# Optimization experiments

Measured on AMD Instinct MI355X. Metric: run time of the kernel, lower is better.

Reference implementation:

```python
import jax, jax.numpy as jnp
import numpy as np

P = 7            # cfg.POOLING_SIZE (= group_size)
N_CLASSES = 21   # PASCAL VOC incl. background
SPATIAL_SCALE = 1.0 / 16.0


def _round_half_up(x):
    # matches C round() for non-negative roi coords (jnp.round is banker's)
    return jnp.floor(x + 0.5)


def psroi_pool(feat, rois, out_dim):
    """Position-sensitive RoI average pooling via integral images.
    feat: [B, out_dim*P*P, H, W]; rois: [N, 5] (batch_idx, x1, y1, x2, y2).
    Returns [N, out_dim, P, P]."""
    B, C, H, W = feat.shape
    # summed-area table, zero-padded: S[b,c,h,w] = sum feat[b,c,:h,:w]
    S = jnp.cumsum(jnp.cumsum(feat, axis=2), axis=3)
    S = jnp.pad(S, ((0, 0), (0, 0), (1, 0), (1, 0)))

    b = rois[:, 0].astype(jnp.int32)
    x1 = _round_half_up(rois[:, 1]) * SPATIAL_SCALE
    y1 = _round_half_up(rois[:, 2]) * SPATIAL_SCALE
    x2 = _round_half_up(rois[:, 3] + 1.0) * SPATIAL_SCALE
    y2 = _round_half_up(rois[:, 4] + 1.0) * SPATIAL_SCALE
    roi_w = jnp.maximum(x2 - x1, 0.1)
    roi_h = jnp.maximum(y2 - y1, 0.1)
    bin_w = roi_w / P
    bin_h = roi_h / P

    g = jnp.arange(P, dtype=feat.dtype)
    hs = jnp.clip(jnp.floor(g[None] * bin_h[:, None] + y1[:, None]), 0, H).astype(jnp.int32)        # [N,P]
    he = jnp.clip(jnp.ceil((g[None] + 1.0) * bin_h[:, None] + y1[:, None]), 0, H).astype(jnp.int32)
    ws = jnp.clip(jnp.floor(g[None] * bin_w[:, None] + x1[:, None]), 0, W).astype(jnp.int32)
    we = jnp.clip(jnp.ceil((g[None] + 1.0) * bin_w[:, None] + x1[:, None]), 0, W).astype(jnp.int32)

    # channel for (ctop, gh, gw) is (ctop*P + gh)*P + gw == arange(C) reshaped
    c = jnp.arange(C, dtype=jnp.int32).reshape(1, out_dim, P, P)
    bi = b[:, None, None, None]
    h0 = hs[:, None, :, None]; h1 = he[:, None, :, None]
    w0 = ws[:, None, None, :]; w1 = we[:, None, None, :]
    # box-sum from integral image -> [N, out_dim, P, P]
    ssum = S[bi, c, h1, w1] - S[bi, c, h0, w1] - S[bi, c, h1, w0] + S[bi, c, h0, w0]

    dh = jnp.maximum(he - hs, 0)[:, None, :, None]
    dw = jnp.maximum(we - ws, 0)[:, None, None, :]
    area = (dh * dw).astype(feat.dtype)
    return jnp.where(area > 0, ssum / jnp.maximum(area, 1.0), 0.0)


def setup_inputs() -> dict:
    key = jax.random.key(0)
    k1, k2, k3, k4, k5 = jax.random.split(key, 5)
    B, Cin, H, W = 4, 2048, 64, 64
    base_feat = jax.random.normal(k1, (B, Cin, H, W), jnp.float32)
    w_conv1 = 0.01 * jax.random.normal(k2, (1024, Cin), jnp.float32)
    w_cls = 0.01 * jax.random.normal(k3, (N_CLASSES * P * P, 1024), jnp.float32)
    w_bbox = 0.001 * jax.random.normal(k4, (4 * N_CLASSES * P * P, 1024), jnp.float32)
    # 300 ROIs per image in image coords (image size = 16*H = 1024)
    n_per = 300
    ka, kb = jax.random.split(k5)
    xy1 = jax.random.uniform(ka, (B * n_per, 2), jnp.float32, 0.0, 900.0)
    wh = jax.random.uniform(kb, (B * n_per, 2), jnp.float32, 16.0, 160.0)
    xy2 = jnp.minimum(xy1 + wh, 1023.0)
    bidx = jnp.repeat(jnp.arange(B, dtype=jnp.float32), n_per)[:, None]
    rois = jnp.concatenate([bidx, xy1[:, 0:1], xy1[:, 1:2], xy2[:, 0:1], xy2[:, 1:2]], axis=1)
    return {"base_feat": base_feat, "rois": rois, "w_conv1": w_conv1, "w_cls": w_cls, "w_bbox": w_bbox}


def reference(base_feat, rois, w_conv1, w_cls, w_bbox):
    B = base_feat.shape[0]
    n_per = rois.shape[0] // B
    # 1x1 conv (no bias) + relu
    x = jax.nn.relu(jnp.einsum('oi,bihw->bohw', w_conv1, base_feat))
    # cls branch: 1x1 conv -> PSRoIPool -> PxP avgpool -> softmax
    cls_feat = jnp.einsum('oi,bihw->bohw', w_cls, x)
    pooled_cls = psroi_pool(cls_feat, rois, N_CLASSES)        # [N, 21, P, P]
    cls_score = pooled_cls.mean(axis=(2, 3))                   # [N, 21]
    cls_prob = jax.nn.softmax(cls_score, axis=1)
    # bbox branch: 1x1 conv -> PSRoIPool -> PxP avgpool
    bbox_feat = jnp.einsum('oi,bihw->bohw', w_bbox, x)
    pooled_loc = psroi_pool(bbox_feat, rois, 4 * N_CLASSES)    # [N, 84, P, P]
    bbox_pred = pooled_loc.mean(axis=(2, 3))                    # [N, 84]
    return cls_prob.reshape(B, n_per, -1), bbox_pred.reshape(B, n_per, -1)
```

## Files before the change

kernel.cpp:

```cpp
#include <hip/hip_runtime.h>
#include <cstdint>


typedef __attribute__((ext_vector_type(8))) short short8;
typedef __attribute__((ext_vector_type(4))) short short4v;
typedef __attribute__((ext_vector_type(4))) float f32x4;

#define OFF_FEATT 0ull
#define OFF_W1    67108864ull
#define OFF_U2    0ull
#define OFF_P2    64225280ull
#define OFF_WC    71303168ull
#define OFF_DESC  84148224ull
#define OFF_SCORE 86155264ull
#define OFF_X     86810624ull
#define OFF_U1    153919488ull
#define OFF_P1    282370048ull
#define ONEPASS_BYTES 296419328ull

__device__ __forceinline__ unsigned short f2bf(float f) {
  unsigned u = __float_as_uint(f);
  u += 0x7fffu + ((u >> 16) & 1u);
  return (unsigned short)(u >> 16);
}
__device__ __forceinline__ float bf2f(unsigned short h) {
  return __uint_as_float(((unsigned)h) << 16);
}

__device__ __forceinline__ int swz6(int k6, int key) {
  return ((((k6 >> 3) & 7) ^ key) << 3) | (k6 & 7);
}

__device__ __forceinline__ void gload16(const void* g, void* l) {
  __builtin_amdgcn_global_load_lds((const __attribute__((address_space(1))) void*)g,
                                   (__attribute__((address_space(3))) void*)l, 16, 0, 0);
}

__global__ __launch_bounds__(256) void k_cvt_w1(const float* __restrict__ src,
                                                unsigned short* __restrict__ dst) {
  int t = blockIdx.x * 256 + threadIdx.x;
  long e = (long)t * 4;
  if (e >= 1024 * 2048) return;
  int o = (int)(e >> 11), k = (int)(e & 2047);
  float4 q = *(const float4*)(src + e);
  short4v s = {(short)f2bf(q.x), (short)f2bf(q.y), (short)f2bf(q.z), (short)f2bf(q.w)};
  int kp = (k & ~63) | swz6(k & 63, o & 7);
  *(short4v*)(dst + (size_t)o * 2048 + kp) = s;
}

__global__ __launch_bounds__(256) void k_cvt_wcomb(const float* __restrict__ wcls,
                                                   const float* __restrict__ wbbox,
                                                   unsigned short* __restrict__ dst) {
  int t = blockIdx.x * 256 + threadIdx.x;
  if (t >= 128 * 49 * 256) return;
  size_t e = (size_t)t * 4;
  int c = (int)(e / 50176);
  int rem = (int)(e - (size_t)c * 50176);
  int ij = rem >> 10, k = rem & 1023;
  float4 q = make_float4(0.f, 0.f, 0.f, 0.f);
  if (c < 21)       q = *(const float4*)(wcls + (size_t)(c * 49 + ij) * 1024 + k);
  else if (c < 105) q = *(const float4*)(wbbox + (size_t)((c - 21) * 49 + ij) * 1024 + k);
  short4v s = {(short)f2bf(q.x), (short)f2bf(q.y), (short)f2bf(q.z), (short)f2bf(q.w)};
  int kp = (k & ~63) | swz6(k & 63, c & 7);
  *(short4v*)(dst + ((size_t)(c * 49 + ij) * 1024 + kp)) = s;
}

__global__ __launch_bounds__(256) void k_tpose(const float* __restrict__ src,
                                               unsigned short* __restrict__ dst) {
  __shared__ float tile[64][65];
  int s0 = blockIdx.x * 64, c0 = blockIdx.y * 64, b = blockIdx.z;
  int tx = threadIdx.x & 63, ty = threadIdx.x >> 6;
  const float* sp = src + ((size_t)b * 2048 + c0) * 4096 + s0;
#pragma unroll
  for (int i = 0; i < 16; i++) {
    int cl = ty * 16 + i;
    tile[cl][tx] = sp[(size_t)cl * 4096 + tx];
  }
  __syncthreads();
  unsigned short* dp = dst + ((size_t)b * 4096 + s0) * 2048 + c0;
  int c4 = (threadIdx.x & 15) * 4;
  int sy = threadIdx.x >> 4;
#pragma unroll
  for (int i = 0; i < 4; i++) {
    int sl = i * 16 + sy;
    int key = sl & 7;
    short4v v = {(short)f2bf(tile[c4 + 0][sl]), (short)f2bf(tile[c4 + 1][sl]),
                 (short)f2bf(tile[c4 + 2][sl]), (short)f2bf(tile[c4 + 3][sl])};
    *(short4v*)(dp + (size_t)sl * 2048 + swz6(c4, key)) = v;
  }
}

__global__ __launch_bounds__(256) void k_gemm_conv1(const short* __restrict__ A,
                                                    const short* __restrict__ Bw,
                                                    float* __restrict__ X) {
  int mt = blockIdx.x, nt = blockIdx.y, b = blockIdx.z;
  __shared__ short As[128 * 64];
  __shared__ short Bs[128 * 64];
  int tid = threadIdx.x, lane = tid & 63, wave = tid >> 6;
  int wm = wave >> 1, wn = wave & 1;
  f32x4 acc[4][4];
#pragma unroll
  for (int i = 0; i < 4; i++)
#pragma unroll
    for (int j = 0; j < 4; j++) acc[i][j] = (f32x4){0.f, 0.f, 0.f, 0.f};

  const short* Ab = A + ((size_t)b * 4096 + (size_t)mt * 128) * 2048;
  const short* Bb = Bw + (size_t)nt * 128 * 2048;
  int lr = lane >> 3;
  int lc = (lane & 7) * 8;
  int key = lane & 7;

  for (int k0 = 0; k0 < 2048; k0 += 64) {
#pragma unroll
    for (int i = 0; i < 4; i++) {
      int row = i * 32 + wave * 8 + lr;
      gload16(Ab + (size_t)row * 2048 + k0 + lc, (char*)As + (i * 32 + wave * 8) * 128);
      gload16(Bb + (size_t)row * 2048 + k0 + lc, (char*)Bs + (i * 32 + wave * 8) * 128);
    }
    __syncthreads();
#pragma unroll
    for (int kt = 0; kt < 2; kt++) {
      int ko = (((kt << 2) | (lane >> 4)) ^ key) << 3;
      short8 af[4], bfr[4];
#pragma unroll
      for (int i = 0; i < 4; i++)
        af[i] = *(const short8*)(As + (wm * 64 + i * 16 + (lane & 15)) * 64 + ko);
#pragma unroll
      for (int j = 0; j < 4; j++)
        bfr[j] = *(const short8*)(Bs + (wn * 64 + j * 16 + (lane & 15)) * 64 + ko);
#pragma unroll
      for (int i = 0; i < 4; i++)
#pragma unroll
        for (int j = 0; j < 4; j++)
          acc[i][j] = __builtin_amdgcn_mfma_f32_16x16x32_bf16(af[i], bfr[j], acc[i][j], 0, 0, 0);
    }
    __syncthreads();
  }
  float* Xb = X + ((size_t)b * 4096 + (size_t)mt * 128) * 1024 + nt * 128;
#pragma unroll
  for (int i = 0; i < 4; i++)
#pragma unroll
    for (int j = 0; j < 4; j++) {
      int row = wm * 64 + i * 16 + (lane >> 4) * 4;
      int col = wn * 64 + j * 16 + (lane & 15);
#pragma unroll
      for (int r = 0; r < 4; r++)
        Xb[(size_t)(row + r) * 1024 + col] = fmaxf(acc[i][j][r], 0.f);
    }
}

__global__ __launch_bounds__(256) void k_desc(const float* __restrict__ rois,
                                              int* __restrict__ desc) {
  int t = blockIdx.x * 256 + threadIdx.x;
  if (t >= 1280 * 49) return;
  int roi = t / 49, ij = t - roi * 49;
  int* d = desc + (size_t)t * 8;
  if (roi >= 1200) { d[0] = 0; d[1] = 0; d[2] = 0; d[3] = 0; d[4] = 0; ((float*)d)[5] = 0.f; return; }
  const float* r = rois + (size_t)roi * 5;
  int b = (int)r[0];
  float x1 = __fmul_rn(floorf(__fadd_rn(r[1], 0.5f)), 0.0625f);
  float y1 = __fmul_rn(floorf(__fadd_rn(r[2], 0.5f)), 0.0625f);
  float x2 = __fmul_rn(floorf(__fadd_rn(__fadd_rn(r[3], 1.0f), 0.5f)), 0.0625f);
  float y2 = __fmul_rn(floorf(__fadd_rn(__fadd_rn(r[4], 1.0f), 0.5f)), 0.0625f);
  float bw = __fdiv_rn(fmaxf(__fsub_rn(x2, x1), 0.1f), 7.0f);
  float bh = __fdiv_rn(fmaxf(__fsub_rn(y2, y1), 0.1f), 7.0f);
  int i = ij / 7, j = ij - (ij / 7) * 7;
  float fi = (float)i, fj = (float)j;
  int hs = (int)fminf(fmaxf(floorf(__fadd_rn(__fmul_rn(fi, bh), y1)), 0.f), 64.f);
  int he = (int)fminf(fmaxf(ceilf(__fadd_rn(__fmul_rn(__fadd_rn(fi, 1.f), bh), y1)), 0.f), 64.f);
  int wsx = (int)fminf(fmaxf(floorf(__fadd_rn(__fmul_rn(fj, bw), x1)), 0.f), 64.f);
  int we = (int)fminf(fmaxf(ceilf(__fadd_rn(__fmul_rn(__fadd_rn(fj, 1.f), bw), x1)), 0.f), 64.f);
  int dh = max(he - hs, 0), dw = max(we - wsx, 0);
  float inv = (dh * dw > 0) ? 1.0f / (float)(dh * dw) : 0.f;
  d[0] = b; d[1] = hs; d[2] = he; d[3] = wsx; d[4] = we;
  ((float*)d)[5] = inv;
}

__global__ __launch_bounds__(256) void k_ubuild(const float* __restrict__ X,
                                                const int* __restrict__ desc,
                                                unsigned short* __restrict__ U) {
  int t = blockIdx.x;
  const int* d = desc + (size_t)t * 8;
  int b = d[0], hs = d[1], he = d[2], wsx = d[3], we = d[4];
  float inv = ((const float*)d)[5];
  int key = (t / 49) & 7;
  int k = threadIdx.x * 4;
  float ax = 0.f, ay = 0.f, az = 0.f, aw = 0.f;
  for (int h = hs; h < he; h++) {
    const float* rowp = X + ((size_t)((b * 64 + h) * 64 + wsx)) * 1024 + k;
    for (int w = wsx; w < we; w++) {
      float4 q = *(const float4*)rowp;
      ax += q.x; ay += q.y; az += q.z; aw += q.w;
      rowp += 1024;
    }
  }
  short4v s = {(short)f2bf(ax * inv), (short)f2bf(ay * inv),
               (short)f2bf(az * inv), (short)f2bf(aw * inv)};
  int kp = (k & ~63) | swz6(k & 63, key);
  *(short4v*)(U + (size_t)t * 1024 + kp) = s;
}

__global__ __launch_bounds__(256) void k_poolgemm2(const unsigned short* __restrict__ U,
                                                   const unsigned short* __restrict__ Wc,
                                                   unsigned short* __restrict__ P,
                                                   int nroi) {
  int mt = blockIdx.x;
  int ij = blockIdx.y;
  __shared__ short As[64 * 64];
  __shared__ short Bs[128 * 64];
  int tid = threadIdx.x, lane = tid & 63, wave = tid >> 6;
  f32x4 acc[4][2];
#pragma unroll
  for (int i = 0; i < 4; i++)
#pragma unroll
    for (int j = 0; j < 2; j++) acc[i][j] = (f32x4){0.f, 0.f, 0.f, 0.f};

  const unsigned short* Ab = U + ((size_t)mt * 64 * 49 + ij) * 1024;
  const unsigned short* Bb = Wc + (size_t)ij * 1024;
  int lr = lane >> 3, lc = (lane & 7) * 8;
  int key = lane & 7;

  for (int k0 = 0; k0 < 1024; k0 += 64) {
#pragma unroll
    for (int i = 0; i < 2; i++) {
      int row = i * 32 + wave * 8 + lr;
      gload16(Ab + (size_t)row * (49 * 1024) + k0 + lc, (char*)As + (i * 32 + wave * 8) * 128);
    }
#pragma unroll
    for (int i = 0; i < 4; i++) {
      int row = i * 32 + wave * 8 + lr;
      gload16(Bb + (size_t)row * (49 * 1024) + k0 + lc, (char*)Bs + (i * 32 + wave * 8) * 128);
    }
    __syncthreads();
#pragma unroll
    for (int kt = 0; kt < 2; kt++) {
      int ko = (((kt << 2) | (lane >> 4)) ^ key) << 3;
      short8 af[4], bfr[2];
#pragma unroll
      for (int i = 0; i < 4; i++)
        af[i] = *(const short8*)(As + (i * 16 + (lane & 15)) * 64 + ko);
#pragma unroll
      for (int j = 0; j < 2; j++)
        bfr[j] = *(const short8*)(Bs + (wave * 32 + j * 16 + (lane & 15)) * 64 + ko);
#pragma unroll
      for (int i = 0; i < 4; i++)
#pragma unroll
        for (int j = 0; j < 2; j++)
          acc[i][j] = __builtin_amdgcn_mfma_f32_16x16x32_bf16(af[i], bfr[j], acc[i][j], 0, 0, 0);
    }
    __syncthreads();
  }
  unsigned short* Pb = P + (size_t)ij * nroi * 112;
#pragma unroll
  for (int i = 0; i < 4; i++)
#pragma unroll
    for (int j = 0; j < 2; j++) {
      int cc = wave * 32 + j * 16 + (lane & 15);
      if (cc < 112) {
        int rbase = mt * 64 + i * 16 + (lane >> 4) * 4;
#pragma unroll
        for (int r = 0; r < 4; r++)
          Pb[(size_t)(rbase + r) * 112 + cc] = f2bf(acc[i][j][r]);
      }
    }
}

__global__ __launch_bounds__(256) void k_reduce(const unsigned short* __restrict__ P,
                                                float* __restrict__ score, int nroi) {
  int t = blockIdx.x * 256 + threadIdx.x;
  if (t >= nroi * 112) return;
  int roi = t / 112, c = t - roi * 112;
  float s = 0.f;
#pragma unroll 7
  for (int ij = 0; ij < 49; ij++) s += bf2f(P[(size_t)ij * nroi * 112 + t]);
  score[(size_t)roi * 128 + c] = s;
}

__global__ __launch_bounds__(256) void k_final(const float* __restrict__ score,
                                               float* __restrict__ out) {
  int t = blockIdx.x * 256 + threadIdx.x;
  if (t < 1200) {
    float s[21];
    float mx = -1e30f;
#pragma unroll
    for (int c = 0; c < 21; c++) {
      s[c] = score[(size_t)t * 128 + c] * (1.f / 49.f);
      mx = fmaxf(mx, s[c]);
    }
    float sum = 0.f;
#pragma unroll
    for (int c = 0; c < 21; c++) { s[c] = expf(s[c] - mx); sum += s[c]; }
    float rs = 1.f / sum;
#pragma unroll
    for (int c = 0; c < 21; c++) out[(size_t)t * 21 + c] = s[c] * rs;
  }
  if (t < 100800) {
    int roi = t / 84, c = t - (t / 84) * 84;
    out[25200 + t] = score[(size_t)roi * 128 + 21 + c] * (1.f / 49.f);
  }
}

extern "C" void kernel_launch(void* const* d_in, const int* in_sizes, int n_in,
                              void* d_out, int out_size, void* d_ws, size_t ws_size,
                              hipStream_t stream) {
  const float* base_feat = (const float*)d_in[0];
  const float* rois      = (const float*)d_in[1];
  const float* w_conv1   = (const float*)d_in[2];
  const float* w_cls     = (const float*)d_in[3];
  const float* w_bbox    = (const float*)d_in[4];
  float* out = (float*)d_out;
  char* ws = (char*)d_ws;

  unsigned short* featT = (unsigned short*)(ws + OFF_FEATT);
  unsigned short* w1b   = (unsigned short*)(ws + OFF_W1);
  unsigned short* Wc    = (unsigned short*)(ws + OFF_WC);
  int*            desc  = (int*)(ws + OFF_DESC);
  float*          score = (float*)(ws + OFF_SCORE);
  float*          X     = (float*)(ws + OFF_X);

  k_cvt_w1<<<2048, 256, 0, stream>>>(w_conv1, w1b);
  k_cvt_wcomb<<<6272, 256, 0, stream>>>(w_cls, w_bbox, Wc);
  k_tpose<<<dim3(64, 32, 4), 256, 0, stream>>>(base_feat, featT);
  k_gemm_conv1<<<dim3(32, 8, 4), 256, 0, stream>>>((const short*)featT, (const short*)w1b, X);
  k_desc<<<245, 256, 0, stream>>>(rois, desc);

  if (ws_size >= ONEPASS_BYTES) {
    unsigned short* U = (unsigned short*)(ws + OFF_U1);
    unsigned short* P = (unsigned short*)(ws + OFF_P1);
    k_ubuild<<<1280 * 49, 256, 0, stream>>>(X, desc, U);
    k_poolgemm2<<<dim3(20, 49), 256, 0, stream>>>(U, Wc, P, 1280);
    k_reduce<<<560, 256, 0, stream>>>(P, score, 1280);
  } else {
    unsigned short* U = (unsigned short*)(ws + OFF_U2);
    unsigned short* P = (unsigned short*)(ws + OFF_P2);
    for (int h = 0; h < 2; h++) {
      k_ubuild<<<640 * 49, 256, 0, stream>>>(X, desc + (size_t)h * 640 * 49 * 8, U);
      k_poolgemm2<<<dim3(10, 49), 256, 0, stream>>>(U, Wc, P, 640);
      k_reduce<<<280, 256, 0, stream>>>(P, score + (size_t)h * 640 * 128, 640);
    }
  }
  k_final<<<394, 256, 0, stream>>>(score, out);
}
```

Before: 434.6 us.

## Fuse RoI bin gathering into pool GEMM and merge prep kernels

Removes the separate U buffer: the pool GEMM now gathers and averages X over each RoI bin directly into a double-buffered LDS A tile, and prefetches the next weight tile while gathering. The three small prep kernels (weight conversions, descriptor build) merge into one launch, and the two-pass fallback path is dropped. This avoids writing and re-reading a large bf16 intermediate and cuts launch count. The cost is a longer-latency gather inside the GEMM loop, with lower occupancy from doubled LDS, and each thread now does scattered gathers.

```diff
diff --git a/kernel.cpp b/kernel.cpp
--- a/kernel.cpp
+++ b/kernel.cpp
@@ -7,16 +7,12 @@
 typedef __attribute__((ext_vector_type(4))) float f32x4;
 
 #define OFF_FEATT 0ull
+#define OFF_P     0ull
 #define OFF_W1    67108864ull
-#define OFF_U2    0ull
-#define OFF_P2    64225280ull
 #define OFF_WC    71303168ull
 #define OFF_DESC  84148224ull
 #define OFF_SCORE 86155264ull
 #define OFF_X     86810624ull
-#define OFF_U1    153919488ull
-#define OFF_P1    282370048ull
-#define ONEPASS_BYTES 296419328ull
 
 __device__ __forceinline__ unsigned short f2bf(float f) {
   unsigned u = __float_as_uint(f);
@@ -36,122 +32,37 @@
                                    (__attribute__((address_space(3))) void*)l, 16, 0, 0);
 }
 
-__global__ __launch_bounds__(256) void k_cvt_w1(const float* __restrict__ src,
-                                                unsigned short* __restrict__ dst) {
-  int t = blockIdx.x * 256 + threadIdx.x;
-  long e = (long)t * 4;
-  if (e >= 1024 * 2048) return;
-  int o = (int)(e >> 11), k = (int)(e & 2047);
-  float4 q = *(const float4*)(src + e);
-  short4v s = {(short)f2bf(q.x), (short)f2bf(q.y), (short)f2bf(q.z), (short)f2bf(q.w)};
-  int kp = (k & ~63) | swz6(k & 63, o & 7);
-  *(short4v*)(dst + (size_t)o * 2048 + kp) = s;
-}
-
-__global__ __launch_bounds__(256) void k_cvt_wcomb(const float* __restrict__ wcls,
-                                                   const float* __restrict__ wbbox,
-                                                   unsigned short* __restrict__ dst) {
-  int t = blockIdx.x * 256 + threadIdx.x;
-  if (t >= 128 * 49 * 256) return;
-  size_t e = (size_t)t * 4;
-  int c = (int)(e / 50176);
-  int rem = (int)(e - (size_t)c * 50176);
-  int ij = rem >> 10, k = rem & 1023;
-  float4 q = make_float4(0.f, 0.f, 0.f, 0.f);
-  if (c < 21)       q = *(const float4*)(wcls + (size_t)(c * 49 + ij) * 1024 + k);
-  else if (c < 105) q = *(const float4*)(wbbox + (size_t)((c - 21) * 49 + ij) * 1024 + k);
-  short4v s = {(short)f2bf(q.x), (short)f2bf(q.y), (short)f2bf(q.z), (short)f2bf(q.w)};
-  int kp = (k & ~63) | swz6(k & 63, c & 7);
-  *(short4v*)(dst + ((size_t)(c * 49 + ij) * 1024 + kp)) = s;
-}
-
-__global__ __launch_bounds__(256) void k_tpose(const float* __restrict__ src,
-                                               unsigned short* __restrict__ dst) {
-  __shared__ float tile[64][65];
-  int s0 = blockIdx.x * 64, c0 = blockIdx.y * 64, b = blockIdx.z;
-  int tx = threadIdx.x & 63, ty = threadIdx.x >> 6;
-  const float* sp = src + ((size_t)b * 2048 + c0) * 4096 + s0;
-#pragma unroll
-  for (int i = 0; i < 16; i++) {
-    int cl = ty * 16 + i;
-    tile[cl][tx] = sp[(size_t)cl * 4096 + tx];
-  }
-  __syncthreads();
-  unsigned short* dp = dst + ((size_t)b * 4096 + s0) * 2048 + c0;
-  int c4 = (threadIdx.x & 15) * 4;
-  int sy = threadIdx.x >> 4;
-#pragma unroll
-  for (int i = 0; i < 4; i++) {
-    int sl = i * 16 + sy;
-    int key = sl & 7;
-    short4v v = {(short)f2bf(tile[c4 + 0][sl]), (short)f2bf(tile[c4 + 1][sl]),
-                 (short)f2bf(tile[c4 + 2][sl]), (short)f2bf(tile[c4 + 3][sl])};
-    *(short4v*)(dp + (size_t)sl * 2048 + swz6(c4, key)) = v;
-  }
-}
-
-__global__ __launch_bounds__(256) void k_gemm_conv1(const short* __restrict__ A,
-                                                    const short* __restrict__ Bw,
-                                                    float* __restrict__ X) {
-  int mt = blockIdx.x, nt = blockIdx.y, b = blockIdx.z;
-  __shared__ short As[128 * 64];
-  __shared__ short Bs[128 * 64];
-  int tid = threadIdx.x, lane = tid & 63, wave = tid >> 6;
-  int wm = wave >> 1, wn = wave & 1;
-  f32x4 acc[4][4];
-#pragma unroll
-  for (int i = 0; i < 4; i++)
-#pragma unroll
-    for (int j = 0; j < 4; j++) acc[i][j] = (f32x4){0.f, 0.f, 0.f, 0.f};
-
-  const short* Ab = A + ((size_t)b * 4096 + (size_t)mt * 128) * 2048;
-  const short* Bb = Bw + (size_t)nt * 128 * 2048;
-  int lr = lane >> 3;
-  int lc = (lane & 7) * 8;
-  int key = lane & 7;
-
-  for (int k0 = 0; k0 < 2048; k0 += 64) {
-#pragma unroll
-    for (int i = 0; i < 4; i++) {
-      int row = i * 32 + wave * 8 + lr;
-      gload16(Ab + (size_t)row * 2048 + k0 + lc, (char*)As + (i * 32 + wave * 8) * 128);
-      gload16(Bb + (size_t)row * 2048 + k0 + lc, (char*)Bs + (i * 32 + wave * 8) * 128);
-    }
-    __syncthreads();
-#pragma unroll
-    for (int kt = 0; kt < 2; kt++) {
-      int ko = (((kt << 2) | (lane >> 4)) ^ key) << 3;
-      short8 af[4], bfr[4];
-#pragma unroll
-      for (int i = 0; i < 4; i++)
-        af[i] = *(const short8*)(As + (wm * 64 + i * 16 + (lane & 15)) * 64 + ko);
-#pragma unroll
-      for (int j = 0; j < 4; j++)
-        bfr[j] = *(const short8*)(Bs + (wn * 64 + j * 16 + (lane & 15)) * 64 + ko);
-#pragma unroll
-      for (int i = 0; i < 4; i++)
-#pragma unroll
-        for (int j = 0; j < 4; j++)
-          acc[i][j] = __builtin_amdgcn_mfma_f32_16x16x32_bf16(af[i], bfr[j], acc[i][j], 0, 0, 0);
-    }
-    __syncthreads();
-  }
-  float* Xb = X + ((size_t)b * 4096 + (size_t)mt * 128) * 1024 + nt * 128;
-#pragma unroll
-  for (int i = 0; i < 4; i++)
-#pragma unroll
-    for (int j = 0; j < 4; j++) {
-      int row = wm * 64 + i * 16 + (lane >> 4) * 4;
-      int col = wn * 64 + j * 16 + (lane & 15);
-#pragma unroll
-      for (int r = 0; r < 4; r++)
-        Xb[(size_t)(row + r) * 1024 + col] = fmaxf(acc[i][j][r], 0.f);
-    }
-}
-
-__global__ __launch_bounds__(256) void k_desc(const float* __restrict__ rois,
+__global__ __launch_bounds__(256) void k_prep(const float* __restrict__ w1,
+                                              const float* __restrict__ wcls,
+                                              const float* __restrict__ wbbox,
+                                              const float* __restrict__ rois,
+                                              unsigned short* __restrict__ w1b,
+                                              unsigned short* __restrict__ Wc,
                                               int* __restrict__ desc) {
-  int t = blockIdx.x * 256 + threadIdx.x;
+  int bid = blockIdx.x;
+  if (bid < 2048) {
+    long e = ((long)bid * 256 + threadIdx.x) * 4;
+    int o = (int)(e >> 11), k = (int)(e & 2047);
+    float4 q = *(const float4*)(w1 + e);
+    short4v s = {(short)f2bf(q.x), (short)f2bf(q.y), (short)f2bf(q.z), (short)f2bf(q.w)};
+    int kp = (k & ~63) | swz6(k & 63, o & 7);
+    *(short4v*)(w1b + (size_t)o * 2048 + kp) = s;
+    return;
+  }
+  if (bid < 8320) {
+    size_t e = ((size_t)(bid - 2048) * 256 + threadIdx.x) * 4;
+    int c = (int)(e / 50176);
+    int rem = (int)(e - (size_t)c * 50176);
+    int ij = rem >> 10, k = rem & 1023;
+    float4 q = make_float4(0.f, 0.f, 0.f, 0.f);
+    if (c < 21)       q = *(const float4*)(wcls + (size_t)(c * 49 + ij) * 1024 + k);
+    else if (c < 105) q = *(const float4*)(wbbox + (size_t)((c - 21) * 49 + ij) * 1024 + k);
+    short4v s = {(short)f2bf(q.x), (short)f2bf(q.y), (short)f2bf(q.z), (short)f2bf(q.w)};
+    int kp = (k & ~63) | swz6(k & 63, c & 7);
+    *(short4v*)(Wc + ((size_t)(c * 49 + ij) * 1024 + kp)) = s;
+    return;
+  }
+  int t = (bid - 8320) * 256 + threadIdx.x;
   if (t >= 1280 * 49) return;
   int roi = t / 49, ij = t - roi * 49;
   int* d = desc + (size_t)t * 8;
@@ -176,81 +87,188 @@
   ((float*)d)[5] = inv;
 }
 
-__global__ __launch_bounds__(256) void k_ubuild(const float* __restrict__ X,
-                                                const int* __restrict__ desc,
-                                                unsigned short* __restrict__ U) {
-  int t = blockIdx.x;
-  const int* d = desc + (size_t)t * 8;
+__global__ __launch_bounds__(256) void k_tpose(const float* __restrict__ src,
+                                               unsigned short* __restrict__ dst) {
+  __shared__ float tile[64][65];
+  int s0 = blockIdx.x * 64, c0 = blockIdx.y * 64, b = blockIdx.z;
+  int tx = threadIdx.x & 63, ty = threadIdx.x >> 6;
+  const float* sp = src + ((size_t)b * 2048 + c0) * 4096 + s0;
+#pragma unroll
+  for (int i = 0; i < 16; i++) {
+    int cl = ty * 16 + i;
+    tile[cl][tx] = sp[(size_t)cl * 4096 + tx];
+  }
+  __syncthreads();
+  unsigned short* dp = dst + ((size_t)b * 4096 + s0) * 2048 + c0;
+  int c4 = (threadIdx.x & 15) * 4;
+  int sy = threadIdx.x >> 4;
+#pragma unroll
+  for (int i = 0; i < 4; i++) {
+    int sl = i * 16 + sy;
+    int key = sl & 7;
+    short4v v = {(short)f2bf(tile[c4 + 0][sl]), (short)f2bf(tile[c4 + 1][sl]),
+                 (short)f2bf(tile[c4 + 2][sl]), (short)f2bf(tile[c4 + 3][sl])};
+    *(short4v*)(dp + (size_t)sl * 2048 + swz6(c4, key)) = v;
+  }
+}
+
+__global__ __launch_bounds__(256) void k_gemm_conv1(const short* __restrict__ A,
+                                                    const short* __restrict__ Bw,
+                                                    float* __restrict__ X) {
+  int mt = blockIdx.x, nt = blockIdx.y, b = blockIdx.z;
+  __shared__ short As[128 * 64];
+  __shared__ short Bs[128 * 64];
+  int tid = threadIdx.x, lane = tid & 63, wave = tid >> 6;
+  int wm = wave >> 1, wn = wave & 1;
+  f32x4 acc[4][4];
+#pragma unroll
+  for (int i = 0; i < 4; i++)
+#pragma unroll
+    for (int j = 0; j < 4; j++) acc[i][j] = (f32x4){0.f, 0.f, 0.f, 0.f};
+
+  const short* Ab = A + ((size_t)b * 4096 + (size_t)mt * 128) * 2048;
+  const short* Bb = Bw + (size_t)nt * 128 * 2048;
+  int lr = lane >> 3;
+  int lc = (lane & 7) * 8;
+  int key = lane & 7;
+
+  for (int k0 = 0; k0 < 2048; k0 += 64) {
+#pragma unroll
+    for (int i = 0; i < 4; i++) {
+      int row = i * 32 + wave * 8 + lr;
+      gload16(Ab + (size_t)row * 2048 + k0 + lc, (char*)As + (i * 32 + wave * 8) * 128);
+      gload16(Bb + (size_t)row * 2048 + k0 + lc, (char*)Bs + (i * 32 + wave * 8) * 128);
+    }
+    __syncthreads();
+#pragma unroll
+    for (int kt = 0; kt < 2; kt++) {
+      int ko = (((kt << 2) | (lane >> 4)) ^ key) << 3;
+      short8 af[4], bfr[4];
+#pragma unroll
+      for (int i = 0; i < 4; i++)
+        af[i] = *(const short8*)(As + (wm * 64 + i * 16 + (lane & 15)) * 64 + ko);
+#pragma unroll
+      for (int j = 0; j < 4; j++)
+        bfr[j] = *(const short8*)(Bs + (wn * 64 + j * 16 + (lane & 15)) * 64 + ko);
+#pragma unroll
+      for (int i = 0; i < 4; i++)
+#pragma unroll
+        for (int j = 0; j < 4; j++)
+          acc[i][j] = __builtin_amdgcn_mfma_f32_16x16x32_bf16(af[i], bfr[j], acc[i][j], 0, 0, 0);
+    }
+    __syncthreads();
+  }
+  float* Xb = X + ((size_t)b * 4096 + (size_t)mt * 128) * 1024 + nt * 128;
+#pragma unroll
+  for (int i = 0; i < 4; i++)
+#pragma unroll
+    for (int j = 0; j < 4; j++) {
+      int row = wm * 64 + i * 16 + (lane >> 4) * 4;
+      int col = wn * 64 + j * 16 + (lane & 15);
+#pragma unroll
+      for (int r = 0; r < 4; r++)
+        Xb[(size_t)(row + r) * 1024 + col] = fmaxf(acc[i][j][r], 0.f);
+    }
+}
+
+__global__ __launch_bounds__(256, 3) void k_poolfused(const float* __restrict__ X,
+                                                      const int* __restrict__ desc,
+                                                      const unsigned short* __restrict__ Wc,
+                                                      unsigned short* __restrict__ P) {
+  int mt = blockIdx.x;
+  int ij = blockIdx.y;
+  __shared__ short As[2][64 * 72];
+  __shared__ short Bs[2][128 * 64];
+  int tid = threadIdx.x, lane = tid & 63, wave = tid >> 6;
+  int r = tid >> 2, q = tid & 3;
+
+  const int* d = desc + ((size_t)(mt * 64 + r) * 49 + ij) * 8;
   int b = d[0], hs = d[1], he = d[2], wsx = d[3], we = d[4];
   float inv = ((const float*)d)[5];
-  int key = (t / 49) & 7;
-  int k = threadIdx.x * 4;
-  float ax = 0.f, ay = 0.f, az = 0.f, aw = 0.f;
-  for (int h = hs; h < he; h++) {
-    const float* rowp = X + ((size_t)((b * 64 + h) * 64 + wsx)) * 1024 + k;
-    for (int w = wsx; w < we; w++) {
-      float4 q = *(const float4*)rowp;
-      ax += q.x; ay += q.y; az += q.z; aw += q.w;
-      rowp += 1024;
-    }
-  }
-  short4v s = {(short)f2bf(ax * inv), (short)f2bf(ay * inv),
-               (short)f2bf(az * inv), (short)f2bf(aw * inv)};
-  int kp = (k & ~63) | swz6(k & 63, key);
-  *(short4v*)(U + (size_t)t * 1024 + kp) = s;
-}
-
-__global__ __launch_bounds__(256) void k_poolgemm2(const unsigned short* __restrict__ U,
-                                                   const unsigned short* __restrict__ Wc,
-                                                   unsigned short* __restrict__ P,
-                                                   int nroi) {
-  int mt = blockIdx.x;
-  int ij = blockIdx.y;
-  __shared__ short As[64 * 64];
-  __shared__ short Bs[128 * 64];
-  int tid = threadIdx.x, lane = tid & 63, wave = tid >> 6;
+  const float* Xq = X + (size_t)q * 16;
+
+  const unsigned short* Bb = Wc + (size_t)ij * 1024 +
+                             (size_t)(wave * 8 + (lane >> 3)) * 49 * 1024 + (lane & 7) * 8;
+  int key = lane & 7;
+
   f32x4 acc[4][2];
 #pragma unroll
   for (int i = 0; i < 4; i++)
 #pragma unroll
     for (int j = 0; j < 2; j++) acc[i][j] = (f32x4){0.f, 0.f, 0.f, 0.f};
 
-  const unsigned short* Ab = U + ((size_t)mt * 64 * 49 + ij) * 1024;
-  const unsigned short* Bb = Wc + (size_t)ij * 1024;
-  int lr = lane >> 3, lc = (lane & 7) * 8;
-  int key = lane & 7;
-
-  for (int k0 = 0; k0 < 1024; k0 += 64) {
-#pragma unroll
-    for (int i = 0; i < 2; i++) {
-      int row = i * 32 + wave * 8 + lr;
-      gload16(Ab + (size_t)row * (49 * 1024) + k0 + lc, (char*)As + (i * 32 + wave * 8) * 128);
-    }
-#pragma unroll
-    for (int i = 0; i < 4; i++) {
-      int row = i * 32 + wave * 8 + lr;
-      gload16(Bb + (size_t)row * (49 * 1024) + k0 + lc, (char*)Bs + (i * 32 + wave * 8) * 128);
+  float s[16];
+
+  auto gather = [&](int k0) {
+#pragma unroll
+    for (int z = 0; z < 16; z++) s[z] = 0.f;
+    for (int h = hs; h < he; h++) {
+      const float* rp = Xq + ((size_t)((b * 64 + h) * 64 + wsx)) * 1024 + k0;
+      for (int w = wsx; w < we; w++) {
+        float4 a0 = *(const float4*)(rp + 0);
+        float4 a1 = *(const float4*)(rp + 4);
+        float4 a2 = *(const float4*)(rp + 8);
+        float4 a3 = *(const float4*)(rp + 12);
+        s[0] += a0.x; s[1] += a0.y; s[2] += a0.z; s[3] += a0.w;
+        s[4] += a1.x; s[5] += a1.y; s[6] += a1.z; s[7] += a1.w;
+        s[8] += a2.x; s[9] += a2.y; s[10] += a2.z; s[11] += a2.w;
+        s[12] += a3.x; s[13] += a3.y; s[14] += a3.z; s[15] += a3.w;
+        rp += 1024;
+      }
+    }
+  };
+  auto writeA = [&](int buf) {
+    short8 v0 = {(short)f2bf(s[0] * inv), (short)f2bf(s[1] * inv),
+                 (short)f2bf(s[2] * inv), (short)f2bf(s[3] * inv),
+                 (short)f2bf(s[4] * inv), (short)f2bf(s[5] * inv),
+                 (short)f2bf(s[6] * inv), (short)f2bf(s[7] * inv)};
+    short8 v1 = {(short)f2bf(s[8] * inv), (short)f2bf(s[9] * inv),
+                 (short)f2bf(s[10] * inv), (short)f2bf(s[11] * inv),
+                 (short)f2bf(s[12] * inv), (short)f2bf(s[13] * inv),
+                 (short)f2bf(s[14] * inv), (short)f2bf(s[15] * inv)};
+    *(short8*)&As[buf][r * 72 + q * 16] = v0;
+    *(short8*)&As[buf][r * 72 + q * 16 + 8] = v1;
+  };
+  auto loadB = [&](int k0, int buf) {
+#pragma unroll
+    for (int i = 0; i < 4; i++)
+      gload16(Bb + (size_t)(i * 32) * 49 * 1024 + k0,
+              (char*)Bs[buf] + (i * 32 + wave * 8) * 128);
+  };
+
+  gather(0);
+  loadB(0, 0);
+  __syncthreads();
+  writeA(0);
+
+  for (int kc = 0; kc < 16; kc++) {
+    int cur = kc & 1;
+    if (kc < 15) {
+      loadB((kc + 1) * 64, cur ^ 1);
+      gather((kc + 1) * 64);
     }
     __syncthreads();
 #pragma unroll
     for (int kt = 0; kt < 2; kt++) {
-      int ko = (((kt << 2) | (lane >> 4)) ^ key) << 3;
+      int ko = kt * 32 + (lane >> 4) * 8;
+      int kob = (((kt << 2) | (lane >> 4)) ^ key) << 3;
       short8 af[4], bfr[2];
 #pragma unroll
       for (int i = 0; i < 4; i++)
-        af[i] = *(const short8*)(As + (i * 16 + (lane & 15)) * 64 + ko);
+        af[i] = *(const short8*)(&As[cur][(i * 16 + (lane & 15)) * 72 + ko]);
 #pragma unroll
       for (int j = 0; j < 2; j++)
-        bfr[j] = *(const short8*)(Bs + (wave * 32 + j * 16 + (lane & 15)) * 64 + ko);
+        bfr[j] = *(const short8*)(&Bs[cur][(wave * 32 + j * 16 + (lane & 15)) * 64 + kob]);
 #pragma unroll
       for (int i = 0; i < 4; i++)
 #pragma unroll
         for (int j = 0; j < 2; j++)
           acc[i][j] = __builtin_amdgcn_mfma_f32_16x16x32_bf16(af[i], bfr[j], acc[i][j], 0, 0, 0);
     }
-    __syncthreads();
-  }
-  unsigned short* Pb = P + (size_t)ij * nroi * 112;
+    if (kc < 15) writeA(cur ^ 1);
+  }
+
+  unsigned short* Pb = P + (size_t)ij * 1280 * 112;
 #pragma unroll
   for (int i = 0; i < 4; i++)
 #pragma unroll
@@ -259,20 +277,20 @@
       if (cc < 112) {
         int rbase = mt * 64 + i * 16 + (lane >> 4) * 4;
 #pragma unroll
-        for (int r = 0; r < 4; r++)
-          Pb[(size_t)(rbase + r) * 112 + cc] = f2bf(acc[i][j][r]);
+        for (int r2 = 0; r2 < 4; r2++)
+          Pb[(size_t)(rbase + r2) * 112 + cc] = f2bf(acc[i][j][r2]);
       }
     }
 }
 
 __global__ __launch_bounds__(256) void k_reduce(const unsigned short* __restrict__ P,
-                                                float* __restrict__ score, int nroi) {
+                                                float* __restrict__ score) {
   int t = blockIdx.x * 256 + threadIdx.x;
-  if (t >= nroi * 112) return;
+  if (t >= 1280 * 112) return;
   int roi = t / 112, c = t - roi * 112;
   float s = 0.f;
 #pragma unroll 7
-  for (int ij = 0; ij < 49; ij++) s += bf2f(P[(size_t)ij * nroi * 112 + t]);
+  for (int ij = 0; ij < 49; ij++) s += bf2f(P[(size_t)ij * 1280 * 112 + t]);
   score[(size_t)roi * 128 + c] = s;
 }
 
@@ -317,27 +335,12 @@
   int*            desc  = (int*)(ws + OFF_DESC);
   float*          score = (float*)(ws + OFF_SCORE);
   float*          X     = (float*)(ws + OFF_X);
-
-  k_cvt_w1<<<2048, 256, 0, stream>>>(w_conv1, w1b);
-  k_cvt_wcomb<<<6272, 256, 0, stream>>>(w_cls, w_bbox, Wc);
+  unsigned short* P     = (unsigned short*)(ws + OFF_P);
+
+  k_prep<<<8565, 256, 0, stream>>>(w_conv1, w_cls, w_bbox, rois, w1b, Wc, desc);
   k_tpose<<<dim3(64, 32, 4), 256, 0, stream>>>(base_feat, featT);
   k_gemm_conv1<<<dim3(32, 8, 4), 256, 0, stream>>>((const short*)featT, (const short*)w1b, X);
-  k_desc<<<245, 256, 0, stream>>>(rois, desc);
-
-  if (ws_size >= ONEPASS_BYTES) {
-    unsigned short* U = (unsigned short*)(ws + OFF_U1);
-    unsigned short* P = (unsigned short*)(ws + OFF_P1);
-    k_ubuild<<<1280 * 49, 256, 0, stream>>>(X, desc, U);
-    k_poolgemm2<<<dim3(20, 49), 256, 0, stream>>>(U, Wc, P, 1280);
-    k_reduce<<<560, 256, 0, stream>>>(P, score, 1280);
-  } else {
-    unsigned short* U = (unsigned short*)(ws + OFF_U2);
-    unsigned short* P = (unsigned short*)(ws + OFF_P2);
-    for (int h = 0; h < 2; h++) {
-      k_ubuild<<<640 * 49, 256, 0, stream>>>(X, desc + (size_t)h * 640 * 49 * 8, U);
-      k_poolgemm2<<<dim3(10, 49), 256, 0, stream>>>(U, Wc, P, 640);
-      k_reduce<<<280, 256, 0, stream>>>(P, score + (size_t)h * 640 * 128, 640);
-    }
-  }
+  k_poolfused<<<dim3(20, 49), 256, 0, stream>>>(X, desc, Wc, P);
+  k_reduce<<<560, 256, 0, stream>>>(P, score);
   k_final<<<394, 256, 0, stream>>>(score, out);
 }
```

Result: slower. 461.0 us (+6.1%).
